# Kernel tuning notes

Hardware: AMD Instinct MI355X
Metric: run time of the kernel (lower is better)

The kernel has to match this reference:

```python
import jax, jax.numpy as jnp
import numpy as np

B = 16
H = 56
W = 56
C = 384
NH = 12
HD = C // NH
WS = 7
SHIFT = 3
N = WS * WS
SCALE = HD ** -0.5
EPS = 1e-3  # keras LayerNormalization default epsilon


def _rel_pos_index():
    coords = np.stack(np.meshgrid(np.arange(WS), np.arange(WS), indexing='ij')).reshape(2, -1)
    rel = (coords[:, :, None] - coords[:, None, :]).transpose(1, 2, 0)
    rel[:, :, 0] += WS - 1
    rel[:, :, 1] += WS - 1
    rel[:, :, 0] *= 2 * WS - 1
    return rel.sum(-1)  # [N, N]

REL_IDX = jnp.asarray(_rel_pos_index())


def _shift_mask():
    # faithful reproduction of the TransformerBlock.__init__ mask construction
    mask = np.zeros((1, H, W, 1), np.float32)
    slices = (slice(0, -WS), slice(-WS, -SHIFT), slice(-SHIFT, None))
    cnt = 0
    for hs in slices:
        for ws in slices:
            mask[:, hs, ws, :] = cnt
            cnt += 1
    mw = mask.reshape(1, H // WS, WS, W // WS, WS, 1).transpose(0, 1, 3, 2, 4, 5).reshape(-1, N)
    m = mw[:, None, :] - mw[:, :, None]  # expand_dims(mw,1) - expand_dims(mw,2)
    return np.where(m != 0, np.float32(-100.0), np.float32(0.0))  # [nw, N, N]

MASK = jnp.asarray(_shift_mask())


def _ln(x, g, b):
    mu = x.mean(-1, keepdims=True)
    var = ((x - mu) ** 2).mean(-1, keepdims=True)
    return (x - mu) / jnp.sqrt(var + EPS) * g + b


def _window_partition(x):  # [B,H,W,C] -> [B*nw, N, C]
    b = x.shape[0]
    x = x.reshape(b, H // WS, WS, W // WS, WS, C).transpose(0, 1, 3, 2, 4, 5)
    return x.reshape(-1, N, C)


def _window_reverse(wins, b):  # [B*nw, WS, WS, C] -> [B,H,W,C]
    x = wins.reshape(b, H // WS, W // WS, WS, WS, C).transpose(0, 1, 3, 2, 4, 5)
    return x.reshape(b, H, W, C)


def setup_inputs() -> dict:
    key = jax.random.key(0)
    ks = jax.random.split(key, 8)
    s = 0.02
    return {
        'x': jax.random.normal(ks[0], (B, H * W, C), jnp.float32),
        'ln1_g': jnp.ones((C,), jnp.float32),
        'ln1_b': jnp.zeros((C,), jnp.float32),
        'ln2_g': jnp.ones((C,), jnp.float32),
        'ln2_b': jnp.zeros((C,), jnp.float32),
        'qkv_w': s * jax.random.normal(ks[1], (C, 3 * C), jnp.float32),
        'qkv_b': jnp.zeros((3 * C,), jnp.float32),
        'proj_w': s * jax.random.normal(ks[2], (C, C), jnp.float32),
        'proj_b': jnp.zeros((C,), jnp.float32),
        'mlp_w1': s * jax.random.normal(ks[3], (C, 4 * C), jnp.float32),
        'mlp_b1': jnp.zeros((4 * C,), jnp.float32),
        'mlp_w2': s * jax.random.normal(ks[4], (4 * C, C), jnp.float32),
        'mlp_b2': jnp.zeros((C,), jnp.float32),
        'rel_pos_table': s * jax.random.normal(ks[5], ((2 * WS - 1) * (2 * WS - 1), NH), jnp.float32),
    }


def reference(x, ln1_g, ln1_b, ln2_g, ln2_b, qkv_w, qkv_b, proj_w, proj_b,
              mlp_w1, mlp_b1, mlp_w2, mlp_b2, rel_pos_table):
    skip = x
    y = _ln(x, ln1_g, ln1_b).reshape(B, H, W, C)
    # cyclic shift (faithful to source: shift=(-s, +s))
    y = jnp.roll(y, shift=(-SHIFT, SHIFT), axis=(1, 2))
    wins = _window_partition(y)                      # [nW, N, C]
    nW = wins.shape[0]

    qkv = wins @ qkv_w + qkv_b                       # [nW, N, 3C]
    qkv = qkv.reshape(nW, N, 3, NH, HD).transpose(2, 0, 3, 1, 4)
    q, k, v = qkv[0] * SCALE, qkv[1], qkv[2]         # [nW, NH, N, HD]

    attn = jnp.einsum('whnd,whmd->whnm', q, k)       # [nW, NH, N, N]
    bias = rel_pos_table[REL_IDX.reshape(-1)].reshape(N, N, NH).transpose(2, 0, 1)
    attn = attn + bias[None]

    nw = MASK.shape[0]
    attn = attn.reshape(nW // nw, nw, NH, N, N) + MASK[None, :, None]
    attn = jax.nn.softmax(attn.reshape(nW, NH, N, N), axis=-1)

    out = jnp.einsum('whnm,whmd->wnhd', attn, v).reshape(nW, N, C)
    out = out @ proj_w + proj_b

    y = _window_reverse(out.reshape(-1, WS, WS, C), B)
    # reverse shift (faithful to source: shift=(+s, +s))
    y = jnp.roll(y, shift=(SHIFT, SHIFT), axis=(1, 2))
    x = y.reshape(B, H * W, C) + skip

    skip = x
    y = _ln(x, ln2_g, ln2_b)
    y = jax.nn.gelu(y @ mlp_w1 + mlp_b1, approximate=False)
    y = y @ mlp_w2 + mlp_b2
    return y + skip
```

## Files before the change

### kernel.cpp

```cpp
#include <hip/hip_runtime.h>
#include <hip/hip_bf16.h>
#include <math.h>

typedef __hip_bfloat16 bf16;
typedef unsigned short ushort_t;
typedef __bf16 bf16x8 __attribute__((ext_vector_type(8)));
typedef float f32x4 __attribute__((ext_vector_type(4)));

#define TOKENS 50176
#define CW2 512
#define CROWS2 (CW2 * 49)
#define SCALE_ 0.17677669529663687f

__device__ __forceinline__ float b2f(bf16 v) { return __bfloat162float(v); }
__device__ __forceinline__ bf16  f2b(float v) { return __float2bfloat16(v); }

__device__ __forceinline__ float gelu_f(float v) {
  float x = v * 0.7071067811865475f;
  float ax = fabsf(x);
  float t = 1.f / (1.f + 0.3275911f * ax);
  float poly = ((((1.061405429f * t - 1.453152027f) * t + 1.421413741f) * t
                 - 0.284496736f) * t + 0.254829592f) * t;
  float erfv = 1.f - poly * __expf(-ax * ax);
  erfv = copysignf(erfv, x);
  return 0.5f * v * (1.f + erfv);
}

__global__ __launch_bounds__(256) void wt_bf16(const float* __restrict__ W,
                                               ushort_t* __restrict__ Wt,
                                               int K, int N) {
  int idx = blockIdx.x * 256 + threadIdx.x;
  if (idx >= K * N) return;
  int n = idx / K, k = idx - n * K;
  bf16 h = f2b(W[(size_t)k * N + n]);
  Wt[idx] = *(ushort_t*)&h;
}

__global__ __launch_bounds__(64) void ln1_kernel(const float* __restrict__ x,
                                                 const float* __restrict__ g,
                                                 const float* __restrict__ bta,
                                                 bf16* __restrict__ wins) {
  int t = blockIdx.x;
  int lane = threadIdx.x;
  int w = t / 49, n = t - w * 49;
  int bi = w >> 6, wi = w & 63;
  int hw = wi >> 3, ww = wi & 7;
  int ti = n / 7, tj = n - ti * 7;
  int hr = hw * 7 + ti, wr = ww * 7 + tj;
  int hs = (hr + 3) % 56;
  int wsc = (wr + 53) % 56;
  const float* row = x + ((size_t)bi * 3136 + hs * 56 + wsc) * 384;
  float v[6];
  float s = 0.f, s2 = 0.f;
#pragma unroll
  for (int j = 0; j < 6; ++j) {
    v[j] = row[lane + 64 * j];
    s += v[j]; s2 += v[j] * v[j];
  }
#pragma unroll
  for (int m = 32; m >= 1; m >>= 1) {
    s  += __shfl_xor(s, m, 64);
    s2 += __shfl_xor(s2, m, 64);
  }
  float mu = s * (1.f / 384.f);
  float var = s2 * (1.f / 384.f) - mu * mu;
  float rstd = rsqrtf(var + 1e-3f);
  bf16* orow = wins + (size_t)t * 384;
#pragma unroll
  for (int j = 0; j < 6; ++j) {
    int c = lane + 64 * j;
    orow[c] = f2b((v[j] - mu) * rstd * g[c] + bta[c]);
  }
}

__global__ __launch_bounds__(64) void ln2_kernel(const float* __restrict__ x1,
                                                 const float* __restrict__ g,
                                                 const float* __restrict__ bta,
                                                 bf16* __restrict__ out) {
  int t = blockIdx.x;
  int lane = threadIdx.x;
  const float* row = x1 + (size_t)t * 384;
  float v[6];
  float s = 0.f, s2 = 0.f;
#pragma unroll
  for (int j = 0; j < 6; ++j) {
    v[j] = row[lane + 64 * j];
    s += v[j]; s2 += v[j] * v[j];
  }
#pragma unroll
  for (int m = 32; m >= 1; m >>= 1) {
    s  += __shfl_xor(s, m, 64);
    s2 += __shfl_xor(s2, m, 64);
  }
  float mu = s * (1.f / 384.f);
  float var = s2 * (1.f / 384.f) - mu * mu;
  float rstd = rsqrtf(var + 1e-3f);
  bf16* orow = out + (size_t)t * 384;
#pragma unroll
  for (int j = 0; j < 6; ++j) {
    int c = lane + 64 * j;
    orow[c] = f2b((v[j] - mu) * rstd * g[c] + bta[c]);
  }
}

template<int MODE>
__global__ __launch_bounds__(256) void mfma_gemm(
    const ushort_t* __restrict__ A, const ushort_t* __restrict__ Bt,
    const float* __restrict__ bias, int N, int K,
    const float* __restrict__ resid, void* __restrict__ out_) {
  __shared__ ushort_t As[128 * 64];
  __shared__ ushort_t Bs[128 * 64];
  int tid = threadIdx.x;
  int lane = tid & 63, wv = tid >> 6;
  int wm = wv >> 1, wn = wv & 1;
  int lm = lane & 15, kg = lane >> 4;
  int row0 = blockIdx.x * 128, col0 = blockIdx.y * 128;
  f32x4 acc[4][4];
#pragma unroll
  for (int i = 0; i < 4; ++i)
#pragma unroll
    for (int j = 0; j < 4; ++j) acc[i][j] = (f32x4){0.f, 0.f, 0.f, 0.f};

  int rsub = lane >> 3;
  int bblk = lane & 7;
  int bs = bblk ^ rsub;

  for (int k0 = 0; k0 < K; k0 += 64) {
#pragma unroll
    for (int ch = 0; ch < 4; ++ch) {
      int r8 = wv * 32 + ch * 8;
      int r = r8 + rsub;
      const ushort_t* ga = &A[(size_t)(row0 + r) * K + k0 + bs * 8];
      const ushort_t* gb = &Bt[(size_t)(col0 + r) * K + k0 + bs * 8];
      __builtin_amdgcn_global_load_lds(
          (const __attribute__((address_space(1))) void*)ga,
          (__attribute__((address_space(3))) void*)&As[r8 * 64], 16, 0, 0);
      __builtin_amdgcn_global_load_lds(
          (const __attribute__((address_space(1))) void*)gb,
          (__attribute__((address_space(3))) void*)&Bs[r8 * 64], 16, 0, 0);
    }
    __syncthreads();
#pragma unroll
    for (int kk = 0; kk < 2; ++kk) {
      bf16x8 a[4], b[4];
#pragma unroll
      for (int i = 0; i < 4; ++i) {
        int ra = wm * 64 + i * 16 + lm;
        int rb = wn * 64 + i * 16 + lm;
        a[i] = *(const bf16x8*)&As[ra * 64 + (((kk * 4 + kg) ^ (ra & 7)) << 3)];
        b[i] = *(const bf16x8*)&Bs[rb * 64 + (((kk * 4 + kg) ^ (rb & 7)) << 3)];
      }
#pragma unroll
      for (int i = 0; i < 4; ++i)
#pragma unroll
        for (int j = 0; j < 4; ++j)
          acc[i][j] = __builtin_amdgcn_mfma_f32_16x16x32_bf16(a[i], b[j], acc[i][j], 0, 0, 0);
    }
    __syncthreads();
  }

  int m0 = row0 + wm * 64, n0 = col0 + wn * 64;
#pragma unroll
  for (int i = 0; i < 4; ++i) {
#pragma unroll
    for (int reg = 0; reg < 4; ++reg) {
      int m = m0 + i * 16 + kg * 4 + reg;
      size_t obase = 0;
      if (MODE == 1) {
        int w = m / 49, nn = m - w * 49;
        int bi = w >> 6, wi = w & 63;
        int hw = wi >> 3, ww = wi & 7;
        int ti = nn / 7, tj = nn - ti * 7;
        int hf = (hw * 7 + ti + 3) % 56, wf = (ww * 7 + tj + 3) % 56;
        obase = ((size_t)bi * 3136 + hf * 56 + wf) * 384;
      }
#pragma unroll
      for (int j = 0; j < 4; ++j) {
        int cN = n0 + j * 16 + lm;
        float v = acc[i][j][reg] + bias[cN];
        if (MODE == 0) {
          ((bf16*)out_)[(size_t)m * N + cN] = f2b(v);
        } else if (MODE == 1) {
          float* O = (float*)out_;
          O[obase + cN] = v + resid[obase + cN];
        } else if (MODE == 2) {
          ((bf16*)out_)[(size_t)m * N + cN] = f2b(gelu_f(v));
        } else {
          float* O = (float*)out_;
          O[(size_t)m * N + cN] = v + resid[(size_t)m * N + cN];
        }
      }
    }
  }
}

__global__ __launch_bounds__(256) void attn_mfma(const ushort_t* __restrict__ qkv_c,
                                                 const float* __restrict__ table,
                                                 ushort_t* __restrict__ attn_c,
                                                 int w_base) {
  int wl = blockIdx.x >> 2, hg = blockIdx.x & 3;
  int w = w_base + wl;
  int wi = w & 63;
  int hw = wi >> 3, ww = wi & 7;
  __shared__ ushort_t Qs[64 * 40];
  __shared__ ushort_t Ks[64 * 40];
  __shared__ ushort_t Vt[32 * 72];
  __shared__ ushort_t Ps[64 * 72];
  __shared__ float bias_s[169 * 12];
  int tid = threadIdx.x;
  int lane = tid & 63, wv = tid >> 6;
  int lm = lane & 15, kg = lane >> 4;

  for (int i = tid; i < 64 * 40; i += 256) { Qs[i] = 0; Ks[i] = 0; }
  for (int i = tid; i < 32 * 72; i += 256) Vt[i] = 0;
  for (int i = tid; i < 169 * 12; i += 256) bias_s[i] = table[i];
  __syncthreads();

  for (int hh = 0; hh < 3; ++hh) {
    int h = hg * 3 + hh;
    const ushort_t* base = qkv_c + (size_t)wl * 49 * 1152 + h * 32;
    for (int idx = tid; idx < 392; idx += 256) {
      int n = idx >> 3, d0 = (idx & 7) * 4;
      const ushort_t* p = base + (size_t)n * 1152 + d0;
      ushort4 q = *(const ushort4*)(p);
      ushort4 k = *(const ushort4*)(p + 384);
      ushort4 v = *(const ushort4*)(p + 768);
      *(ushort4*)&Qs[n * 40 + d0] = q;
      *(ushort4*)&Ks[n * 40 + d0] = k;
      Vt[(d0 + 0) * 72 + n] = v.x;
      Vt[(d0 + 1) * 72 + n] = v.y;
      Vt[(d0 + 2) * 72 + n] = v.z;
      Vt[(d0 + 3) * 72 + n] = v.w;
    }
    __syncthreads();

    bf16x8 qa = *(const bf16x8*)&Qs[(wv * 16 + lm) * 40 + kg * 8];
    f32x4 sacc[4];
#pragma unroll
    for (int jt = 0; jt < 4; ++jt) {
      bf16x8 kb = *(const bf16x8*)&Ks[(jt * 16 + lm) * 40 + kg * 8];
      sacc[jt] = __builtin_amdgcn_mfma_f32_16x16x32_bf16(
          qa, kb, (f32x4){0.f, 0.f, 0.f, 0.f}, 0, 0, 0);
    }

    int i_base = wv * 16 + kg * 4;
#pragma unroll
    for (int reg = 0; reg < 4; ++reg) {
      int i = i_base + reg;
      int ii = (i < 49) ? i : 0;
      int yi = ii / 7, xi = ii - yi * 7;
      int hri = hw * 7 + yi, wri = ww * 7 + xi;
      int ri = (hri < 49 ? 0 : (hri < 53 ? 1 : 2)) * 3 + (wri < 49 ? 0 : (wri < 53 ? 1 : 2));
      float sv[4];
      float mx = -1e30f;
#pragma unroll
      for (int jt = 0; jt < 4; ++jt) {
        int j = jt * 16 + lm;
        int jj = (j < 49) ? j : 0;
        int yj = jj / 7, xj = jj - yj * 7;
        int hrj = hw * 7 + yj, wrj = ww * 7 + xj;
        int rj = (hrj < 49 ? 0 : (hrj < 53 ? 1 : 2)) * 3 + (wrj < 49 ? 0 : (wrj < 53 ? 1 : 2));
        int ridx = (yi - yj + 6) * 13 + (xi - xj + 6);
        float s = sacc[jt][reg] * SCALE_ + bias_s[ridx * 12 + h] + ((ri == rj) ? 0.f : -100.f);
        sv[jt] = (j < 49) ? s : -1e30f;
        mx = fmaxf(mx, sv[jt]);
      }
#pragma unroll
      for (int msk = 1; msk < 16; msk <<= 1) mx = fmaxf(mx, __shfl_xor(mx, msk, 64));
      float sm = 0.f;
#pragma unroll
      for (int jt = 0; jt < 4; ++jt) {
        float e = ((jt * 16 + lm) < 49) ? __expf(sv[jt] - mx) : 0.f;
        sv[jt] = e; sm += e;
      }
#pragma unroll
      for (int msk = 1; msk < 16; msk <<= 1) sm += __shfl_xor(sm, msk, 64);
      float inv = 1.f / sm;
#pragma unroll
      for (int jt = 0; jt < 4; ++jt) {
        bf16 pb = f2b(sv[jt] * inv);
        Ps[(size_t)i * 72 + jt * 16 + lm] = *(ushort_t*)&pb;
      }
    }
    f32x4 oacc[2] = {(f32x4){0.f, 0.f, 0.f, 0.f}, (f32x4){0.f, 0.f, 0.f, 0.f}};
#pragma unroll
    for (int ks = 0; ks < 2; ++ks) {
      bf16x8 pa = *(const bf16x8*)&Ps[(wv * 16 + lm) * 72 + ks * 32 + kg * 8];
#pragma unroll
      for (int dt = 0; dt < 2; ++dt) {
        bf16x8 vb = *(const bf16x8*)&Vt[(dt * 16 + lm) * 72 + ks * 32 + kg * 8];
        oacc[dt] = __builtin_amdgcn_mfma_f32_16x16x32_bf16(pa, vb, oacc[dt], 0, 0, 0);
      }
    }
#pragma unroll
    for (int reg = 0; reg < 4; ++reg) {
      int r = i_base + reg;
      if (r < 49) {
#pragma unroll
        for (int dt = 0; dt < 2; ++dt) {
          bf16 ob = f2b(oacc[dt][reg]);
          attn_c[((size_t)wl * 49 + r) * 384 + h * 32 + dt * 16 + lm] = *(ushort_t*)&ob;
        }
      }
    }
    __syncthreads();
  }
}

extern "C" void kernel_launch(void* const* d_in, const int* in_sizes, int n_in,
                              void* d_out, int out_size, void* d_ws, size_t ws_size,
                              hipStream_t stream) {
  const float* x      = (const float*)d_in[0];
  const float* ln1_g  = (const float*)d_in[1];
  const float* ln1_b  = (const float*)d_in[2];
  const float* ln2_g  = (const float*)d_in[3];
  const float* ln2_b  = (const float*)d_in[4];
  const float* qkv_w  = (const float*)d_in[5];
  const float* qkv_b  = (const float*)d_in[6];
  const float* proj_w = (const float*)d_in[7];
  const float* proj_b = (const float*)d_in[8];
  const float* mlp_w1 = (const float*)d_in[9];
  const float* mlp_b1 = (const float*)d_in[10];
  const float* mlp_w2 = (const float*)d_in[11];
  const float* mlp_b2 = (const float*)d_in[12];
  const float* rel_tb = (const float*)d_in[13];

  char* ws = (char*)d_ws;
  ushort_t* r0 = (ushort_t*)(ws + 0);
  ushort_t* r1 = (ushort_t*)(ws + 38535168ull);
  ushort_t* wq = (ushort_t*)(ws + 115605504ull);
  ushort_t* wp = wq + 442368;
  ushort_t* w1 = wp + 147456;
  ushort_t* w2 = w1 + 589824;
  float* out = (float*)d_out;

  wt_bf16<<<1728, 256, 0, stream>>>(qkv_w, wq, 384, 1152);
  wt_bf16<<<576, 256, 0, stream>>>(proj_w, wp, 384, 384);
  wt_bf16<<<2304, 256, 0, stream>>>(mlp_w1, w1, 384, 1536);
  wt_bf16<<<2304, 256, 0, stream>>>(mlp_w2, w2, 1536, 384);

  ln1_kernel<<<TOKENS, 64, 0, stream>>>(x, ln1_g, ln1_b, (bf16*)r0);

  for (int c = 0; c < 2; ++c) {
    ushort_t* winc = r0 + (size_t)c * CROWS2 * 384;
    mfma_gemm<0><<<dim3(CROWS2 / 128, 9), 256, 0, stream>>>(
        winc, wq, qkv_b, 1152, 384, nullptr, (void*)r1);
    attn_mfma<<<CW2 * 4, 256, 0, stream>>>(r1, rel_tb, winc, c * CW2);
  }

  mfma_gemm<1><<<dim3(TOKENS / 128, 3), 256, 0, stream>>>(
      r0, wp, proj_b, 384, 384, x, (void*)out);

  ln2_kernel<<<TOKENS, 64, 0, stream>>>(out, ln2_g, ln2_b, (bf16*)r0);

  for (int c = 0; c < 2; ++c) {
    ushort_t* lc = r0 + (size_t)c * CROWS2 * 384;
    float* oc = out + (size_t)c * CROWS2 * 384;
    mfma_gemm<2><<<dim3(CROWS2 / 128, 12), 256, 0, stream>>>(
        lc, w1, mlp_b1, 1536, 384, nullptr, (void*)r1);
    mfma_gemm<3><<<dim3(CROWS2 / 128, 3), 256, 0, stream>>>(
        r1, w2, mlp_b2, 384, 1536, oc, (void*)oc);
  }
}
```

Before: 702.5 us.

## Double-buffer GEMM LDS tiles with BK=32 and swap grid order for A-tile reuse

The MFMA GEMM now uses two LDS buffers with a K-step of 32. It issues the async global-to-LDS load for the next tile before computing on the current one, so memory latency overlaps with MFMA work, and it needs only one barrier per step. The grid is also transposed so that consecutive blocks share the same row tile of A, which should improve L2 reuse of activations. The costs are half the work per barrier and a new swizzle pattern that could cause LDS bank conflicts.

```diff
diff --git a/kernel.cpp b/kernel.cpp
--- a/kernel.cpp
+++ b/kernel.cpp
@@ -108,55 +108,62 @@
     const ushort_t* __restrict__ A, const ushort_t* __restrict__ Bt,
     const float* __restrict__ bias, int N, int K,
     const float* __restrict__ resid, void* __restrict__ out_) {
-  __shared__ ushort_t As[128 * 64];
-  __shared__ ushort_t Bs[128 * 64];
+  __shared__ ushort_t As[2][128 * 32];
+  __shared__ ushort_t Bs[2][128 * 32];
   int tid = threadIdx.x;
   int lane = tid & 63, wv = tid >> 6;
   int wm = wv >> 1, wn = wv & 1;
   int lm = lane & 15, kg = lane >> 4;
-  int row0 = blockIdx.x * 128, col0 = blockIdx.y * 128;
+  int col0 = blockIdx.x * 128, row0 = blockIdx.y * 128;
   f32x4 acc[4][4];
 #pragma unroll
   for (int i = 0; i < 4; ++i)
 #pragma unroll
     for (int j = 0; j < 4; ++j) acc[i][j] = (f32x4){0.f, 0.f, 0.f, 0.f};
 
-  int rsub = lane >> 3;
-  int bblk = lane & 7;
-  int bs = bblk ^ rsub;
-
-  for (int k0 = 0; k0 < K; k0 += 64) {
-#pragma unroll
-    for (int ch = 0; ch < 4; ++ch) {
-      int r8 = wv * 32 + ch * 8;
-      int r = r8 + rsub;
-      const ushort_t* ga = &A[(size_t)(row0 + r) * K + k0 + bs * 8];
-      const ushort_t* gb = &Bt[(size_t)(col0 + r) * K + k0 + bs * 8];
+  int rsub = lane >> 2;
+  int bs = (lane & 3) ^ ((rsub >> 1) & 3);
+  int pbr = kg ^ ((lm >> 1) & 3);
+
+  auto stage = [&](int t, int buf) {
+    int kk0 = t << 5;
+#pragma unroll
+    for (int ch = 0; ch < 2; ++ch) {
+      int c = wv * 2 + ch;
+      int r = c * 16 + rsub;
+      const ushort_t* ga = &A[(size_t)(row0 + r) * K + kk0 + bs * 8];
+      const ushort_t* gb = &Bt[(size_t)(col0 + r) * K + kk0 + bs * 8];
       __builtin_amdgcn_global_load_lds(
           (const __attribute__((address_space(1))) void*)ga,
-          (__attribute__((address_space(3))) void*)&As[r8 * 64], 16, 0, 0);
+          (__attribute__((address_space(3))) void*)&As[buf][c * 512], 16, 0, 0);
       __builtin_amdgcn_global_load_lds(
           (const __attribute__((address_space(1))) void*)gb,
-          (__attribute__((address_space(3))) void*)&Bs[r8 * 64], 16, 0, 0);
-    }
+          (__attribute__((address_space(3))) void*)&Bs[buf][c * 512], 16, 0, 0);
+    }
+  };
+
+  int NT = K >> 5;
+  int cur = 0;
+  stage(0, 0);
+  __syncthreads();
+
+  for (int t = 0; t < NT; ++t) {
+    if (t + 1 < NT) stage(t + 1, cur ^ 1);
+    bf16x8 a[4], b[4];
+#pragma unroll
+    for (int i = 0; i < 4; ++i) {
+      int ra = wm * 64 + i * 16 + lm;
+      int rb = wn * 64 + i * 16 + lm;
+      a[i] = *(const bf16x8*)&As[cur][ra * 32 + pbr * 8];
+      b[i] = *(const bf16x8*)&Bs[cur][rb * 32 + pbr * 8];
+    }
+#pragma unroll
+    for (int i = 0; i < 4; ++i)
+#pragma unroll
+      for (int j = 0; j < 4; ++j)
+        acc[i][j] = __builtin_amdgcn_mfma_f32_16x16x32_bf16(a[i], b[j], acc[i][j], 0, 0, 0);
     __syncthreads();
-#pragma unroll
-    for (int kk = 0; kk < 2; ++kk) {
-      bf16x8 a[4], b[4];
-#pragma unroll
-      for (int i = 0; i < 4; ++i) {
-        int ra = wm * 64 + i * 16 + lm;
-        int rb = wn * 64 + i * 16 + lm;
-        a[i] = *(const bf16x8*)&As[ra * 64 + (((kk * 4 + kg) ^ (ra & 7)) << 3)];
-        b[i] = *(const bf16x8*)&Bs[rb * 64 + (((kk * 4 + kg) ^ (rb & 7)) << 3)];
-      }
-#pragma unroll
-      for (int i = 0; i < 4; ++i)
-#pragma unroll
-        for (int j = 0; j < 4; ++j)
-          acc[i][j] = __builtin_amdgcn_mfma_f32_16x16x32_bf16(a[i], b[j], acc[i][j], 0, 0, 0);
-    }
-    __syncthreads();
+    cur ^= 1;
   }
 
   int m0 = row0 + wm * 64, n0 = col0 + wn * 64;
@@ -343,12 +350,12 @@
 
   for (int c = 0; c < 2; ++c) {
     ushort_t* winc = r0 + (size_t)c * CROWS2 * 384;
-    mfma_gemm<0><<<dim3(CROWS2 / 128, 9), 256, 0, stream>>>(
+    mfma_gemm<0><<<dim3(9, CROWS2 / 128), 256, 0, stream>>>(
         winc, wq, qkv_b, 1152, 384, nullptr, (void*)r1);
     attn_mfma<<<CW2 * 4, 256, 0, stream>>>(r1, rel_tb, winc, c * CW2);
   }
 
-  mfma_gemm<1><<<dim3(TOKENS / 128, 3), 256, 0, stream>>>(
+  mfma_gemm<1><<<dim3(3, TOKENS / 128), 256, 0, stream>>>(
       r0, wp, proj_b, 384, 384, x, (void*)out);
 
   ln2_kernel<<<TOKENS, 64, 0, stream>>>(out, ln2_g, ln2_b, (bf16*)r0);
@@ -356,9 +363,9 @@
   for (int c = 0; c < 2; ++c) {
     ushort_t* lc = r0 + (size_t)c * CROWS2 * 384;
     float* oc = out + (size_t)c * CROWS2 * 384;
-    mfma_gemm<2><<<dim3(CROWS2 / 128, 12), 256, 0, stream>>>(
+    mfma_gemm<2><<<dim3(12, CROWS2 / 128), 256, 0, stream>>>(
         lc, w1, mlp_b1, 1536, 384, nullptr, (void*)r1);
-    mfma_gemm<3><<<dim3(CROWS2 / 128, 3), 256, 0, stream>>>(
+    mfma_gemm<3><<<dim3(3, CROWS2 / 128), 256, 0, stream>>>(
         r1, w2, mlp_b2, 384, 1536, oc, (void*)oc);
   }
 }
```

Result: faster. 668.5 us (-4.8%).
